# Kernel optimization log

Hardware: AMD Instinct MI355X
Metric: run time of the kernel (lower is better)

Reference implementation:

```python
import jax, jax.numpy as jnp
import numpy as np

B, C, H, W = 32, 1, 720, 1280


def setup_inputs() -> dict:
    key = jax.random.key(0)
    k1, k2 = jax.random.split(key)
    right_img = jax.random.normal(k1, (B, C, H, W), dtype=jnp.float32)
    # disparity in [0, 64): realistic stereo disparities, some pixels sample out of bounds
    disp = jax.random.uniform(k2, (B, C, H, W), dtype=jnp.float32) * 64.0
    return {"right_img": right_img, "disp": disp}


def _warp(right_img, disp):
    b, c, h, w = right_img.shape
    dt = disp.dtype
    # grid construction (align_corners=True style normalization, as in the module)
    xs = jnp.arange(w, dtype=dt)  # [W]
    ys = jnp.arange(h, dtype=dt)  # [H]
    gx = xs[None, None, :] - disp[:, 0]                      # [B,H,W]
    gx = (gx - (w - 1) / 2) / (w - 1) * 2
    gy = (ys[None, :, None] - (h - 1) / 2) / (h - 1) * 2     # [1,H,1]
    gy = jnp.broadcast_to(gy, gx.shape)                      # [B,H,W]
    # F.grid_sample default: bilinear, align_corners=False, padding_mode='zeros'
    ix = ((gx + 1) * w - 1) / 2
    iy = ((gy + 1) * h - 1) / 2
    x0 = jnp.floor(ix)
    y0 = jnp.floor(iy)
    wx1 = ix - x0
    wy1 = iy - y0
    wx0 = 1.0 - wx1
    wy0 = 1.0 - wy1
    x0i = x0.astype(jnp.int32)
    y0i = y0.astype(jnp.int32)
    x1i = x0i + 1
    y1i = y0i + 1

    def gather(img, yy, xx):  # img [C,H,W]; yy,xx [H,W] -> [C,H,W]
        valid = (xx >= 0) & (xx < w) & (yy >= 0) & (yy < h)
        xc = jnp.clip(xx, 0, w - 1)
        yc = jnp.clip(yy, 0, h - 1)
        return img[:, yc, xc] * valid[None].astype(img.dtype)

    g = jax.vmap(gather)
    v00 = g(right_img, y0i, x0i)
    v01 = g(right_img, y0i, x1i)
    v10 = g(right_img, y1i, x0i)
    v11 = g(right_img, y1i, x1i)
    out = (v00 * (wy0 * wx0)[:, None] + v01 * (wy0 * wx1)[:, None]
           + v10 * (wy1 * wx0)[:, None] + v11 * (wy1 * wx1)[:, None])
    return out  # [B,C,H,W]


def reference(right_img, disp):
    return _warp(right_img, disp)
```

## Files before the change

### kernel.cpp

```cpp
#include <hip/hip_runtime.h>

constexpr int Bn = 32;
constexpr int Hn = 720;
constexpr int Wn = 1280;
constexpr int WIN = 512;

#define GLL(g, l) __builtin_amdgcn_global_load_lds(                         \
    (const __attribute__((address_space(1))) void*)(g),                     \
    (__attribute__((address_space(3))) void*)(l), 16, 0, 0)

__global__ __launch_bounds__(320) void warp_kernel(
    const float* __restrict__ img,
    const float* __restrict__ disp,
    float* __restrict__ out)
{
    __shared__ float srow[5 * 2 * WIN];

    const int blk  = blockIdx.x;
    const int b    = blk / Hn;
    const int y    = blk - b * Hn;
    const int tid  = threadIdx.x;
    const int lane = tid & 63;
    const int wid  = tid >> 6;

    constexpr float sy = (float)Hn / (float)(Hn - 1);
    const float iy  = fmaf((float)y, sy, -0.5f);
    const float fy0 = floorf(iy);
    float wy1 = iy - fy0;
    float wy0 = 1.0f - wy1;
    const int y0 = (int)fy0;
    const int y1 = y0 + 1;
    if (y0 < 0)   wy0 = 0.0f;
    if (y1 >= Hn) wy1 = 0.0f;
    const int y0c = min(max(y0, 0), Hn - 1);
    const int y1c = min(max(y1, 0), Hn - 1);

    const float* imb = img + (long long)b * (Hn * Wn);

    const int xs = wid << 8;
    const int ws = min(max(xs - 128, 0), Wn - WIN);

    float* wv = srow + (wid << 10);
    const float* src0 = imb + y0c * Wn + ws;
    const float* src1 = imb + y1c * Wn + ws;

    GLL(src0 +       (lane << 2), wv +             (lane << 2));
    GLL(src0 + 256 + (lane << 2), wv + 256 +       (lane << 2));
    GLL(src1 +       (lane << 2), wv + WIN +       (lane << 2));
    GLL(src1 + 256 + (lane << 2), wv + WIN + 256 + (lane << 2));

    const int base = blk * Wn + (tid << 2);
    const float4 d4 = *reinterpret_cast<const float4*>(disp + base);

    asm volatile("s_waitcnt vmcnt(0)" ::: "memory");

    constexpr float sx = (float)Wn / (float)(Wn - 1);
    const float xf0 = (float)(tid << 2);
    const float dv[4] = {d4.x, d4.y, d4.z, d4.w};
    float res[4];

#pragma unroll
    for (int i = 0; i < 4; ++i) {
        const float ix  = fmaf(xf0 + (float)i - dv[i], sx, -0.5f);
        const float fx0 = floorf(ix);
        float wx1 = ix - fx0;
        float wx0 = 1.0f - wx1;
        const int x0 = (int)fx0;
        const int x1 = x0 + 1;
        wx0 = ((unsigned)x0 < (unsigned)Wn) ? wx0 : 0.0f;
        wx1 = ((unsigned)x1 < (unsigned)Wn) ? wx1 : 0.0f;
        const int xl0 = min(max(x0, 0), Wn - 1) - ws;
        const int xl1 = min(max(x1, 0), Wn - 1) - ws;

        const float v00 = wv[xl0];
        const float v01 = wv[xl1];
        const float v10 = wv[xl0 + WIN];
        const float v11 = wv[xl1 + WIN];

        const float t0 = v00 * wy0 + v10 * wy1;
        const float t1 = v01 * wy0 + v11 * wy1;
        res[i] = t0 * wx0 + t1 * wx1;
    }

    *reinterpret_cast<float4*>(out + base) =
        make_float4(res[0], res[1], res[2], res[3]);
}

extern "C" void kernel_launch(void* const* d_in, const int* in_sizes, int n_in,
                              void* d_out, int out_size, void* d_ws, size_t ws_size,
                              hipStream_t stream) {
    const float* img  = (const float*)d_in[0];
    const float* disp = (const float*)d_in[1];
    float* out = (float*)d_out;

    const int grid  = Bn * Hn;
    const int block = 320;

    warp_kernel<<<grid, block, 0, stream>>>(img, disp, out);
}
```

Before: 273.7 us.

## Make warp kernel persistent with double-buffered async row staging

Replaces one-block-per-row launch with a persistent grid of 1280 blocks that loop over rows, double-buffering both source image rows and the disparity row in LDS via global_load_lds so loads for the next row overlap compute of the current one. Full rows are staged once and shared by all waves instead of per-wave overlapping windows, removing redundant loads. It adds per-iteration barriers and hand-tuned vmcnt waits, which are fragile, and the fixed grid size may limit occupancy.

```diff
diff --git a/kernel.cpp b/kernel.cpp
--- a/kernel.cpp
+++ b/kernel.cpp
@@ -3,87 +3,118 @@
 constexpr int Bn = 32;
 constexpr int Hn = 720;
 constexpr int Wn = 1280;
-constexpr int WIN = 512;
+constexpr int TOT = Bn * Hn;
+constexpr int GRID = 1280;
+constexpr int BUF  = 3 * Wn;
 
 #define GLL(g, l) __builtin_amdgcn_global_load_lds(                         \
     (const __attribute__((address_space(1))) void*)(g),                     \
     (__attribute__((address_space(3))) void*)(l), 16, 0, 0)
+
+#define WAITV(n) asm volatile("s_waitcnt vmcnt(" #n ")" ::: "memory")
+#define MEMFENCE() asm volatile("" ::: "memory")
 
 __global__ __launch_bounds__(320) void warp_kernel(
     const float* __restrict__ img,
     const float* __restrict__ disp,
     float* __restrict__ out)
 {
-    __shared__ float srow[5 * 2 * WIN];
+    __shared__ float srow[2 * BUF];
 
-    const int blk  = blockIdx.x;
-    const int b    = blk / Hn;
-    const int y    = blk - b * Hn;
     const int tid  = threadIdx.x;
     const int lane = tid & 63;
     const int wid  = tid >> 6;
 
-    constexpr float sy = (float)Hn / (float)(Hn - 1);
-    const float iy  = fmaf((float)y, sy, -0.5f);
-    const float fy0 = floorf(iy);
-    float wy1 = iy - fy0;
-    float wy0 = 1.0f - wy1;
-    const int y0 = (int)fy0;
-    const int y1 = y0 + 1;
-    if (y0 < 0)   wy0 = 0.0f;
-    if (y1 >= Hn) wy1 = 0.0f;
-    const int y0c = min(max(y0, 0), Hn - 1);
-    const int y1c = min(max(y1, 0), Hn - 1);
+    auto stage = [&](float* buf, int t) {
+        const int b = t / Hn;
+        const int y = t - b * Hn;
+        constexpr float sy = (float)Hn / (float)(Hn - 1);
+        const float iy = fmaf((float)y, sy, -0.5f);
+        const int y0 = (int)floorf(iy);
+        const int y1 = y0 + 1;
+        const int y0c = min(max(y0, 0), Hn - 1);
+        const int y1c = min(max(y1, 0), Hn - 1);
+        const float* imb = img + b * (Hn * Wn);
+#pragma unroll
+        for (int k = 0; k < 2; ++k) {
+            const int f = (wid << 9) + (k << 8);
+            const float* src = (f < Wn) ? (imb + y0c * Wn + f)
+                                        : (imb + y1c * Wn + (f - Wn));
+            GLL(src + (lane << 2), buf + f + (lane << 2));
+        }
+        const int g = (wid << 8);
+        GLL(disp + t * Wn + g + (lane << 2), buf + 2 * Wn + g + (lane << 2));
+    };
 
-    const float* imb = img + (long long)b * (Hn * Wn);
+    auto compute = [&](const float* buf, int t) {
+        const int b = t / Hn;
+        const int y = t - b * Hn;
+        constexpr float sy = (float)Hn / (float)(Hn - 1);
+        const float iy  = fmaf((float)y, sy, -0.5f);
+        const float fy0 = floorf(iy);
+        float wy1 = iy - fy0;
+        float wy0 = 1.0f - wy1;
+        const int y0 = (int)fy0;
+        if (y0 < 0)       wy0 = 0.0f;
+        if (y0 + 1 >= Hn) wy1 = 0.0f;
 
-    const int xs = wid << 8;
-    const int ws = min(max(xs - 128, 0), Wn - WIN);
+        const float4 d4 = *reinterpret_cast<const float4*>(buf + 2 * Wn + (tid << 2));
+        const float* r0 = buf;
+        const float* r1 = buf + Wn;
 
-    float* wv = srow + (wid << 10);
-    const float* src0 = imb + y0c * Wn + ws;
-    const float* src1 = imb + y1c * Wn + ws;
+        constexpr float sx = (float)Wn / (float)(Wn - 1);
+        const float xf0 = (float)(tid << 2);
+        const float dv[4] = {d4.x, d4.y, d4.z, d4.w};
+        float res[4];
+#pragma unroll
+        for (int i = 0; i < 4; ++i) {
+            const float ix  = fmaf(xf0 + (float)i - dv[i], sx, -0.5f);
+            const float fx0 = floorf(ix);
+            float wx1 = ix - fx0;
+            float wx0 = 1.0f - wx1;
+            const int x0 = (int)fx0;
+            const int x1 = x0 + 1;
+            wx0 = ((unsigned)x0 < (unsigned)Wn) ? wx0 : 0.0f;
+            wx1 = ((unsigned)x1 < (unsigned)Wn) ? wx1 : 0.0f;
+            const int xl0 = min(max(x0, 0), Wn - 1);
+            const int xl1 = min(max(x1, 0), Wn - 1);
 
-    GLL(src0 +       (lane << 2), wv +             (lane << 2));
-    GLL(src0 + 256 + (lane << 2), wv + 256 +       (lane << 2));
-    GLL(src1 +       (lane << 2), wv + WIN +       (lane << 2));
-    GLL(src1 + 256 + (lane << 2), wv + WIN + 256 + (lane << 2));
+            const float v00 = r0[xl0];
+            const float v01 = r0[xl1];
+            const float v10 = r1[xl0];
+            const float v11 = r1[xl1];
 
-    const int base = blk * Wn + (tid << 2);
-    const float4 d4 = *reinterpret_cast<const float4*>(disp + base);
+            const float t0v = v00 * wy0 + v10 * wy1;
+            const float t1v = v01 * wy0 + v11 * wy1;
+            res[i] = t0v * wx0 + t1v * wx1;
+        }
+        *reinterpret_cast<float4*>(out + t * Wn + (tid << 2)) =
+            make_float4(res[0], res[1], res[2], res[3]);
+    };
 
-    asm volatile("s_waitcnt vmcnt(0)" ::: "memory");
+    const int t0 = blockIdx.x;
+    float* buf0 = srow;
+    float* buf1 = srow + BUF;
 
-    constexpr float sx = (float)Wn / (float)(Wn - 1);
-    const float xf0 = (float)(tid << 2);
-    const float dv[4] = {d4.x, d4.y, d4.z, d4.w};
-    float res[4];
+    stage(buf0, t0);
+    if (t0 + GRID < TOT) stage(buf1, t0 + GRID);
 
-#pragma unroll
-    for (int i = 0; i < 4; ++i) {
-        const float ix  = fmaf(xf0 + (float)i - dv[i], sx, -0.5f);
-        const float fx0 = floorf(ix);
-        float wx1 = ix - fx0;
-        float wx0 = 1.0f - wx1;
-        const int x0 = (int)fx0;
-        const int x1 = x0 + 1;
-        wx0 = ((unsigned)x0 < (unsigned)Wn) ? wx0 : 0.0f;
-        wx1 = ((unsigned)x1 < (unsigned)Wn) ? wx1 : 0.0f;
-        const int xl0 = min(max(x0, 0), Wn - 1) - ws;
-        const int xl1 = min(max(x1, 0), Wn - 1) - ws;
-
-        const float v00 = wv[xl0];
-        const float v01 = wv[xl1];
-        const float v10 = wv[xl0 + WIN];
-        const float v11 = wv[xl1 + WIN];
-
-        const float t0 = v00 * wy0 + v10 * wy1;
-        const float t1 = v01 * wy0 + v11 * wy1;
-        res[i] = t0 * wx0 + t1 * wx1;
+    int p = 0;
+    for (int t = t0; t < TOT; t += GRID, p ^= 1) {
+        const bool hn = (t + GRID) < TOT;
+        const bool hs = (t != t0);
+        if (hn) { if (hs) WAITV(4); else WAITV(3); }
+        else    { if (hs) WAITV(1); else WAITV(0); }
+        __builtin_amdgcn_s_barrier();
+        MEMFENCE();
+        float* buf = (p == 0) ? buf0 : buf1;
+        compute(buf, t);
+        MEMFENCE();
+        __builtin_amdgcn_s_barrier();
+        MEMFENCE();
+        const int t2 = t + 2 * GRID;
+        if (t2 < TOT) stage(buf, t2);
     }
-
-    *reinterpret_cast<float4*>(out + base) =
-        make_float4(res[0], res[1], res[2], res[3]);
 }
 
 extern "C" void kernel_launch(void* const* d_in, const int* in_sizes, int n_in,
@@ -93,8 +124,5 @@
     const float* disp = (const float*)d_in[1];
     float* out = (float*)d_out;
 
-    const int grid  = Bn * Hn;
-    const int block = 320;
-
-    warp_kernel<<<grid, block, 0, stream>>>(img, disp, out);
+    warp_kernel<<<GRID, 320, 0, stream>>>(img, disp, out);
 }
```

Result: slower. 284.0 us (+3.8%).
